# Performance work log

Hardware: AMD Instinct MI355X
Metric: run time of the kernel (lower is better)

The kernel has to match this reference:

```python
import jax, jax.numpy as jnp
import numpy as np

N_NODES = 50000
N_EDGES = 1000000
IN_C = 64
OUT_C = 64
N_TYPES = 4


def setup_inputs() -> dict:
    key = jax.random.key(0)
    k_x, k_ei, k_et, k_w, k_rw, k_rb = jax.random.split(key, 6)
    x = jax.random.normal(k_x, (N_NODES, IN_C), dtype=jnp.float32)
    edge_index = jax.random.randint(k_ei, (2, N_EDGES), 0, N_NODES, dtype=jnp.int64)
    edge_type = jax.random.randint(k_et, (N_EDGES,), 0, N_TYPES, dtype=jnp.int64)
    # xavier_uniform for weight: bound = sqrt(6/(in+out))
    bound_w = float(np.sqrt(6.0 / (IN_C + OUT_C)))
    weight = jax.random.uniform(k_w, (N_TYPES, IN_C, OUT_C), minval=-bound_w, maxval=bound_w, dtype=jnp.float32)
    # nn.Linear default init: kaiming_uniform-ish, U(-1/sqrt(in), 1/sqrt(in))
    bound_l = float(1.0 / np.sqrt(IN_C))
    root_w = jax.random.uniform(k_rw, (IN_C, OUT_C), minval=-bound_l, maxval=bound_l, dtype=jnp.float32)
    root_b = jax.random.uniform(k_rb, (OUT_C,), minval=-bound_l, maxval=bound_l, dtype=jnp.float32)
    return {"x": x, "edge_index": edge_index, "edge_type": edge_type,
            "weight": weight, "root_w": root_w, "root_b": root_b}


def reference(x, edge_index, edge_type, weight, root_w, root_b):
    src, dst = edge_index[0], edge_index[1]
    x_src = x[src]                                   # [E, in]
    # Per-type GEMM + masked select; avoids materializing weight[edge_type] ([E,in,out]).
    msgs = jnp.zeros((x_src.shape[0], weight.shape[2]), dtype=x.dtype)
    for t in range(weight.shape[0]):                 # small fixed type count
        sel = (edge_type == t)[:, None]
        msgs = msgs + jnp.where(sel, x_src @ weight[t], 0.0)
    # Scatter-add messages to destination nodes.
    agg = jax.ops.segment_sum(msgs, dst, num_segments=x.shape[0])  # [N, out]
    return agg + x @ root_w + root_b
```

## Files before the change

kernel.cpp:

```cpp
#include <hip/hip_runtime.h>

#define NT 64
#define NBMAX 4096
#define CAPB 2048
#define FILLB 256

typedef short bf16x8 __attribute__((ext_vector_type(8)));
typedef float f32x4  __attribute__((ext_vector_type(4)));

__device__ __forceinline__ unsigned short f2bf(float f) {
    unsigned u = __builtin_bit_cast(unsigned, f);
    unsigned r = (u + 0x7fffu + ((u >> 16) & 1u)) >> 16;
    return (unsigned short)r;
}
__device__ __forceinline__ float bf2f(unsigned short h) {
    return __builtin_bit_cast(float, (unsigned)h << 16);
}
__device__ __forceinline__ unsigned pack2(float a, float b) {
    return (unsigned)f2bf(a) | ((unsigned)f2bf(b) << 16);
}

__global__ __launch_bounds__(256) void prep_w_kernel(
    const float* __restrict__ weight, const float* __restrict__ root_w,
    unsigned short* __restrict__ wt, int* __restrict__ cursor, int nb)
{
    int g = blockIdx.x * 256 + threadIdx.x;
    if (g <= nb) cursor[g] = 0;
    if (g >= 5 * 4096) return;
    int m = g >> 12, rem = g & 4095, c = rem >> 6, k = rem & 63;
    float v = (m < 4) ? weight[m * 4096 + k * 64 + c] : root_w[k * 64 + c];
    int byte = m * 8192 + c * 128 + ((k * 2) ^ ((c & 7) << 4));
    wt[byte >> 1] = f2bf(v);
}

__global__ __launch_bounds__(256) void fused_fg_kernel(
    const float* __restrict__ x, const uint4* __restrict__ wt4,
    const float* __restrict__ root_b,
    float* __restrict__ out, unsigned short* __restrict__ y, int n_nodes,
    const int* __restrict__ ei, const int* __restrict__ et,
    int* __restrict__ cursor, int* __restrict__ spill,
    unsigned* __restrict__ payload, int n_edges, int nb, int ssh, int tsh)
{
    __shared__ __align__(16) char smem[49152];
    const int tid = threadIdx.x;

    if (blockIdx.x < FILLB) {
        int* lh    = (int*)smem;
        int* lbase = lh + NBMAX;
        const int chunk = (n_edges + FILLB - 1) / FILLB;
        const int lo = blockIdx.x * chunk;
        const int hi = min(lo + chunk, n_edges);
        for (int i = tid; i < nb; i += 256) lh[i] = 0;
        __syncthreads();
        for (int e = lo + tid; e < hi; e += 256)
            atomicAdd(&lh[ei[n_edges + e] >> 6], 1);
        __syncthreads();
        for (int i = tid; i < nb; i += 256) {
            int c = lh[i];
            lbase[i] = c ? atomicAdd(&cursor[i], c) : 0;
            lh[i] = 0;
        }
        __syncthreads();
        for (int e = lo + tid; e < hi; e += 256) {
            int src = ei[e];
            int d   = ei[n_edges + e];
            int t   = et[e];
            int b   = d >> 6;
            int r   = atomicAdd(&lh[b], 1);
            int pos = lbase[b] + r;
            if (pos < CAPB) {
                payload[(size_t)b * CAPB + pos] =
                    (unsigned)src | ((unsigned)(d & 63) << ssh) | ((unsigned)t << tsh);
            } else {
                int sp = atomicAdd(&cursor[nb], 1);
                spill[sp] = e;
            }
        }
        return;
    }

    uint4* lds4 = (uint4*)smem;
    const int node0 = (blockIdx.x - FILLB) * 64;

    for (int i = tid; i < 2560; i += 256) lds4[512 + i] = wt4[i];

    {
        int n    = tid >> 2;
        int kq   = tid & 3;
        int node = node0 + n;
        uint4 p0, p1;
        if (node < n_nodes) {
            const float4* src = reinterpret_cast<const float4*>(x)
                                + (size_t)node * 16 + kq * 4;
            float4 f0 = src[0], f1 = src[1], f2 = src[2], f3 = src[3];
            p0.x = pack2(f0.x, f0.y); p0.y = pack2(f0.z, f0.w);
            p0.z = pack2(f1.x, f1.y); p0.w = pack2(f1.z, f1.w);
            p1.x = pack2(f2.x, f2.y); p1.y = pack2(f2.z, f2.w);
            p1.z = pack2(f3.x, f3.y); p1.w = pack2(f3.z, f3.w);
        } else {
            p0 = make_uint4(0, 0, 0, 0);
            p1 = p0;
        }
        int s0 = (kq * 2) ^ (n & 7);
        lds4[n * 8 + s0]       = p0;
        lds4[n * 8 + (s0 ^ 1)] = p1;
    }
    __syncthreads();

    const int wv = tid >> 6;
    const int l  = tid & 63;
    const int lo = l & 15;
    const int hi = l >> 4;

    const int arow = wv * 16 + lo;
    bf16x8 a0 = *reinterpret_cast<const bf16x8*>(
        &lds4[arow * 8 + ((0 + hi) ^ (arow & 7))]);
    bf16x8 a1 = *reinterpret_cast<const bf16x8*>(
        &lds4[arow * 8 + ((4 + hi) ^ (arow & 7))]);

    for (int m = 0; m < 5; ++m) {
        f32x4 acc[4];
        #pragma unroll
        for (int ct = 0; ct < 4; ++ct)
            acc[ct] = (f32x4){0.f, 0.f, 0.f, 0.f};

        #pragma unroll
        for (int ct = 0; ct < 4; ++ct) {
            int c     = ct * 16 + lo;
            int bbase = 512 + m * 512 + c * 8;
            bf16x8 b0 = *reinterpret_cast<const bf16x8*>(
                &lds4[bbase + ((0 + hi) ^ (c & 7))]);
            acc[ct] = __builtin_amdgcn_mfma_f32_16x16x32_bf16(a0, b0, acc[ct], 0, 0, 0);
            bf16x8 b1 = *reinterpret_cast<const bf16x8*>(
                &lds4[bbase + ((4 + hi) ^ (c & 7))]);
            acc[ct] = __builtin_amdgcn_mfma_f32_16x16x32_bf16(a1, b1, acc[ct], 0, 0, 0);
        }

        if (m < 4) {
            unsigned short* __restrict__ ym = y + (size_t)m * n_nodes * 64;
            #pragma unroll
            for (int ct = 0; ct < 4; ++ct) {
                int col = ct * 16 + lo;
                #pragma unroll
                for (int r = 0; r < 4; ++r) {
                    int node = node0 + wv * 16 + hi * 4 + r;
                    if (node < n_nodes)
                        ym[(size_t)node * 64 + col] = f2bf(acc[ct][r]);
                }
            }
        } else {
            #pragma unroll
            for (int ct = 0; ct < 4; ++ct) {
                int col = ct * 16 + lo;
                float rb = root_b[col];
                #pragma unroll
                for (int r = 0; r < 4; ++r) {
                    int node = node0 + wv * 16 + hi * 4 + r;
                    if (node < n_nodes)
                        out[(size_t)node * 64 + col] = acc[ct][r] + rb;
                }
            }
        }
    }
}

__global__ __launch_bounds__(1024) void gatherb3_kernel(
    const int* __restrict__ cursor, const unsigned* __restrict__ payload,
    const int* __restrict__ spill, const int* __restrict__ ei,
    const int* __restrict__ et,
    const unsigned short* __restrict__ y, float* __restrict__ out,
    int n_nodes, int n_edges, int nb, int ssh, int tsh)
{
    __shared__ unsigned raw[CAPB];
    __shared__ unsigned srt[CAPB];
    __shared__ int hist[64];
    __shared__ int hoff[65];

    const int tid = threadIdx.x;
    const int b   = blockIdx.x;
    const int n_in = min(cursor[b], CAPB);
    const unsigned* __restrict__ pl_base = payload + (size_t)b * CAPB;

    if (tid < 64) hist[tid] = 0;
    __syncthreads();
    for (int i = tid; i < n_in; i += 1024) {
        unsigned pl = pl_base[i];
        raw[i] = pl;
        atomicAdd(&hist[(pl >> ssh) & 63], 1);
    }
    __syncthreads();
    if (tid < 64) {
        int v = hist[tid];
        int s = v;
        #pragma unroll
        for (int d = 1; d < 64; d <<= 1) {
            int u = __shfl_up(s, d, 64);
            if (tid >= d) s += u;
        }
        hoff[tid] = s - v;
        if (tid == 63) hoff[64] = s;
        hist[tid] = 0;
    }
    __syncthreads();
    for (int i = tid; i < n_in; i += 1024) {
        unsigned pl = raw[i];
        int lnode = (pl >> ssh) & 63;
        int r = atomicAdd(&hist[lnode], 1);
        srt[hoff[lnode] + r] = pl;
    }
    __syncthreads();

    const int g    = tid >> 4;
    const int cq   = tid & 15;
    const int node = b * 64 + g;
    const unsigned smask = (1u << ssh) - 1;
    const ushort4* __restrict__ y4 = reinterpret_cast<const ushort4*>(y);

    float4 acc = make_float4(0.f, 0.f, 0.f, 0.f);
    const int s0 = hoff[g];
    const int s1 = hoff[g + 1];
    int p = s0;
    for (; p + 1 < s1; p += 2) {
        unsigned pl0 = srt[p];
        unsigned pl1 = srt[p + 1];
        ushort4 v0 = y4[((long)(pl0 >> tsh) * n_nodes + (pl0 & smask)) * 16 + cq];
        ushort4 v1 = y4[((long)(pl1 >> tsh) * n_nodes + (pl1 & smask)) * 16 + cq];
        acc.x += bf2f(v0.x) + bf2f(v1.x);
        acc.y += bf2f(v0.y) + bf2f(v1.y);
        acc.z += bf2f(v0.z) + bf2f(v1.z);
        acc.w += bf2f(v0.w) + bf2f(v1.w);
    }
    if (p < s1) {
        unsigned pl = srt[p];
        ushort4 v = y4[((long)(pl >> tsh) * n_nodes + (pl & smask)) * 16 + cq];
        acc.x += bf2f(v.x); acc.y += bf2f(v.y);
        acc.z += bf2f(v.z); acc.w += bf2f(v.w);
    }

    const int S = cursor[nb];
    for (int i = 0; i < S; ++i) {
        int e = spill[i];
        int d = ei[n_edges + e];
        if ((d >> 6) == b && (d & 63) == g) {
            int src = ei[e];
            int t   = et[e];
            ushort4 v = y4[((long)t * n_nodes + src) * 16 + cq];
            acc.x += bf2f(v.x); acc.y += bf2f(v.y);
            acc.z += bf2f(v.z); acc.w += bf2f(v.w);
        }
    }

    if (node < n_nodes) {
        float4* o  = reinterpret_cast<float4*>(out) + (long)node * 16 + cq;
        float4 cur = *o;
        cur.x += acc.x; cur.y += acc.y; cur.z += acc.z; cur.w += acc.w;
        *o = cur;
    }
}

__global__ __launch_bounds__(256) void gemm_fused2_kernel(
    const float* __restrict__ x, const float* __restrict__ weight,
    const float* __restrict__ root_w, const float* __restrict__ root_b,
    float* __restrict__ out, unsigned short* __restrict__ y, int n_nodes)
{
    __shared__ unsigned short xsT[64][72];
    __shared__ float ws[64][72];
    const int tid   = threadIdx.x;
    const int node0 = blockIdx.x * 64;
    #pragma unroll
    for (int i = 0; i < 4; ++i) {
        int v    = tid + i * 256;
        int r    = v >> 4;
        int cq   = v & 15;
        int node = node0 + r;
        float4 x4 = (node < n_nodes)
                        ? reinterpret_cast<const float4*>(x)[(size_t)node * 16 + cq]
                        : make_float4(0.f, 0.f, 0.f, 0.f);
        xsT[cq * 4 + 0][r] = f2bf(x4.x);
        xsT[cq * 4 + 1][r] = f2bf(x4.y);
        xsT[cq * 4 + 2][r] = f2bf(x4.z);
        xsT[cq * 4 + 3][r] = f2bf(x4.w);
    }
    const int ng = tid & 31;
    const int cg = tid >> 5;
    float bias[8];
    #pragma unroll
    for (int j = 0; j < 8; ++j) bias[j] = root_b[cg * 8 + j];
    for (int m = 0; m < 5; ++m) {
        const float* __restrict__ W = (m < 4) ? (weight + m * 4096) : root_w;
        __syncthreads();
        #pragma unroll
        for (int i = 0; i < 4; ++i) {
            int v  = tid + i * 256;
            int r  = v >> 4;
            int cq = v & 15;
            float4 w4 = reinterpret_cast<const float4*>(W)[v];
            ws[r][cq * 4 + 0] = w4.x; ws[r][cq * 4 + 1] = w4.y;
            ws[r][cq * 4 + 2] = w4.z; ws[r][cq * 4 + 3] = w4.w;
        }
        __syncthreads();
        float acc[2][8];
        #pragma unroll
        for (int i = 0; i < 2; ++i)
            #pragma unroll
            for (int j = 0; j < 8; ++j) acc[i][j] = 0.f;
        #pragma unroll 4
        for (int k = 0; k < 64; ++k) {
            unsigned xu = *reinterpret_cast<const unsigned*>(&xsT[k][ng * 2]);
            float xv0 = __builtin_bit_cast(float, xu << 16);
            float xv1 = __builtin_bit_cast(float, xu & 0xffff0000u);
            float4 wa = *reinterpret_cast<const float4*>(&ws[k][cg * 8]);
            float4 wb = *reinterpret_cast<const float4*>(&ws[k][cg * 8 + 4]);
            float wv[8] = {wa.x, wa.y, wa.z, wa.w, wb.x, wb.y, wb.z, wb.w};
            #pragma unroll
            for (int j = 0; j < 8; ++j) {
                acc[0][j] += xv0 * wv[j];
                acc[1][j] += xv1 * wv[j];
            }
        }
        #pragma unroll
        for (int i = 0; i < 2; ++i) {
            int node = node0 + ng * 2 + i;
            if (node >= n_nodes) continue;
            if (m < 4) {
                uint4 o;
                o.x = pack2(acc[i][0], acc[i][1]);
                o.y = pack2(acc[i][2], acc[i][3]);
                o.z = pack2(acc[i][4], acc[i][5]);
                o.w = pack2(acc[i][6], acc[i][7]);
                *reinterpret_cast<uint4*>(
                    &y[((size_t)m * n_nodes + node) * 64 + cg * 8]) = o;
            } else {
                float4 oa = make_float4(acc[i][0] + bias[0], acc[i][1] + bias[1],
                                        acc[i][2] + bias[2], acc[i][3] + bias[3]);
                float4 ob = make_float4(acc[i][4] + bias[4], acc[i][5] + bias[5],
                                        acc[i][6] + bias[6], acc[i][7] + bias[7]);
                reinterpret_cast<float4*>(&out[(size_t)node * 64 + cg * 8])[0] = oa;
                reinterpret_cast<float4*>(&out[(size_t)node * 64 + cg * 8])[1] = ob;
            }
        }
    }
}

__global__ __launch_bounds__(256) void scatter_kernel(
    const int* __restrict__ ei, const int* __restrict__ et,
    const unsigned short* __restrict__ y, float* __restrict__ out,
    int n_edges, int n_nodes)
{
    long idx = (long)blockIdx.x * blockDim.x + threadIdx.x;
    if (idx >= (long)n_edges * 16) return;
    int e  = (int)(idx >> 4);
    int cq = (int)(idx & 15);
    int src  = ei[e];
    int dstn = ei[n_edges + e];
    int t    = et[e];
    ushort4 v = reinterpret_cast<const ushort4*>(y)[((long)t * n_nodes + src) * 16 + cq];
    float* o = out + (long)dstn * 64 + cq * 4;
    atomicAdd(o + 0, bf2f(v.x));
    atomicAdd(o + 1, bf2f(v.y));
    atomicAdd(o + 2, bf2f(v.z));
    atomicAdd(o + 3, bf2f(v.w));
}

__global__ __launch_bounds__(256) void gemm_root_kernel(
    const float* __restrict__ x, const float* __restrict__ root_w,
    const float* __restrict__ root_b, float* __restrict__ out, int n_nodes)
{
    __shared__ float xs[NT][65];
    __shared__ float ws[64][65];
    const int tid   = threadIdx.x;
    const int node0 = blockIdx.x * NT;
    #pragma unroll
    for (int i = 0; i < 4; ++i) {
        int v  = tid + i * 256;
        int r  = v >> 4;
        int cq = v & 15;
        float4 w4 = reinterpret_cast<const float4*>(root_w)[v];
        ws[r][cq * 4 + 0] = w4.x; ws[r][cq * 4 + 1] = w4.y;
        ws[r][cq * 4 + 2] = w4.z; ws[r][cq * 4 + 3] = w4.w;
        int node = node0 + r;
        float4 x4 = (node < n_nodes)
                        ? reinterpret_cast<const float4*>(x)[node * 16 + cq]
                        : make_float4(0.f, 0.f, 0.f, 0.f);
        xs[r][cq * 4 + 0] = x4.x; xs[r][cq * 4 + 1] = x4.y;
        xs[r][cq * 4 + 2] = x4.z; xs[r][cq * 4 + 3] = x4.w;
    }
    __syncthreads();
    const int tc = (tid & 15) * 4;
    const int tr = (tid >> 4) * 4;
    float acc[4][4];
    #pragma unroll
    for (int i = 0; i < 4; ++i)
        #pragma unroll
        for (int j = 0; j < 4; ++j) acc[i][j] = 0.f;
    #pragma unroll 4
    for (int k = 0; k < 64; ++k) {
        float xv[4], wv[4];
        #pragma unroll
        for (int i = 0; i < 4; ++i) xv[i] = xs[tr + i][k];
        #pragma unroll
        for (int j = 0; j < 4; ++j) wv[j] = ws[k][tc + j];
        #pragma unroll
        for (int i = 0; i < 4; ++i)
            #pragma unroll
            for (int j = 0; j < 4; ++j) acc[i][j] += xv[i] * wv[j];
    }
    #pragma unroll
    for (int i = 0; i < 4; ++i) {
        int node = node0 + tr + i;
        if (node < n_nodes) {
            float4 o = make_float4(acc[i][0] + root_b[tc + 0], acc[i][1] + root_b[tc + 1],
                                   acc[i][2] + root_b[tc + 2], acc[i][3] + root_b[tc + 3]);
            reinterpret_cast<float4*>(out)[node * 16 + (tc >> 2)] = o;
        }
    }
}

__global__ __launch_bounds__(256) void edge_direct_kernel(
    const float* __restrict__ x, const int* __restrict__ ei,
    const int* __restrict__ et, const float* __restrict__ weight,
    float* __restrict__ out, int n_edges)
{
    int gwave  = (int)((blockIdx.x * (long)blockDim.x + threadIdx.x) >> 6);
    int lane   = threadIdx.x & 63;
    int nwaves = (int)(((long)gridDim.x * blockDim.x) >> 6);
    for (int e = gwave; e < n_edges; e += nwaves) {
        int src  = ei[e];
        int dstn = ei[n_edges + e];
        int t    = et[e];
        float xv = x[src * 64 + lane];
        const float* __restrict__ W = weight + t * 4096;
        float acc = 0.f;
        #pragma unroll 8
        for (int k = 0; k < 64; ++k) {
            float xk = __shfl(xv, k);
            acc += xk * W[k * 64 + lane];
        }
        atomicAdd(&out[(long)dstn * 64 + lane], acc);
    }
}

extern "C" void kernel_launch(void* const* d_in, const int* in_sizes, int n_in,
                              void* d_out, int out_size, void* d_ws, size_t ws_size,
                              hipStream_t stream) {
    const float* x      = (const float*)d_in[0];
    const int*   ei     = (const int*)d_in[1];
    const int*   et     = (const int*)d_in[2];
    const float* weight = (const float*)d_in[3];
    const float* root_w = (const float*)d_in[4];
    const float* root_b = (const float*)d_in[5];
    float* out = (float*)d_out;

    const int n_nodes = in_sizes[0] / 64;
    const int n_edges = in_sizes[2];
    const int nb      = (n_nodes + 63) >> 6;

    int ssh = 1;
    while ((1 << ssh) < n_nodes) ++ssh;
    const int tsh = ssh + 6;

    const size_t wt_bytes = 5 * 4096 * sizeof(unsigned short);
    const size_t y_bytes  = (size_t)4 * n_nodes * 64 * sizeof(unsigned short);
    const size_t b_bytes  = wt_bytes + y_bytes +
        ((size_t)nb + 1 + (size_t)nb * CAPB + n_edges) * 4;

    if (nb <= NBMAX && tsh + 2 <= 32 && ws_size >= b_bytes) {
        unsigned short* wt      = (unsigned short*)d_ws;
        unsigned short* y       = (unsigned short*)((char*)d_ws + wt_bytes);
        int*            cursor  = (int*)((char*)d_ws + wt_bytes + y_bytes);
        unsigned*       payload = (unsigned*)(cursor + nb + 1);
        int*            spill   = (int*)(payload + (size_t)nb * CAPB);

        prep_w_kernel<<<80, 256, 0, stream>>>(weight, root_w, wt, cursor, nb);
        fused_fg_kernel<<<FILLB + nb, 256, 0, stream>>>(
            x, (const uint4*)wt, root_b, out, y, n_nodes,
            ei, et, cursor, spill, payload, n_edges, nb, ssh, tsh);
        gatherb3_kernel<<<nb, 1024, 0, stream>>>(
            cursor, payload, spill, ei, et, y, out,
            n_nodes, n_edges, nb, ssh, tsh);
    } else if (ws_size >= y_bytes) {
        unsigned short* y = (unsigned short*)d_ws;
        gemm_fused2_kernel<<<(n_nodes + 63) / 64, 256, 0, stream>>>(
            x, weight, root_w, root_b, out, y, n_nodes);
        long total  = (long)n_edges * 16;
        int  blocks = (int)((total + 255) / 256);
        scatter_kernel<<<blocks, 256, 0, stream>>>(ei, et, y, out, n_edges, n_nodes);
    } else {
        gemm_root_kernel<<<(n_nodes + NT - 1) / NT, 256, 0, stream>>>(
            x, root_w, root_b, out, n_nodes);
        edge_direct_kernel<<<4096, 256, 0, stream>>>(x, ei, et, weight, out, n_edges);
    }
}
```

Before: 66.99 us.

## Split fused fill/GEMM kernel and transpose MFMA operands for vectorized stores

Splits the combined edge-bucketing and per-node GEMM kernel into two separate launches, with the fill kernel now using 512 blocks instead of 256. The GEMM swaps the MFMA operand order so each lane holds four consecutive output columns of one node. That lets the y writes become packed 8-byte stores and the out writes become float4 stores with a vector bias load. The aim is to cut scattered 2-byte and 4-byte global stores and rebalance the fill work, at the cost of an extra kernel launch and losing overlap between fill and GEMM.

```diff
diff --git a/kernel.cpp b/kernel.cpp
--- a/kernel.cpp
+++ b/kernel.cpp
@@ -3,7 +3,6 @@
 #define NT 64
 #define NBMAX 4096
 #define CAPB 2048
-#define FILLB 256
 
 typedef short bf16x8 __attribute__((ext_vector_type(8)));
 typedef float f32x4  __attribute__((ext_vector_type(4)));
@@ -33,54 +32,54 @@
     wt[byte >> 1] = f2bf(v);
 }
 
-__global__ __launch_bounds__(256) void fused_fg_kernel(
+__global__ __launch_bounds__(256) void fillb_kernel(
+    const int* __restrict__ ei, const int* __restrict__ et,
+    int* __restrict__ cursor, int* __restrict__ spill,
+    unsigned* __restrict__ payload,
+    int n_edges, int nb, int ssh, int tsh)
+{
+    __shared__ int lh[NBMAX];
+    __shared__ int lbase[NBMAX];
+    const int chunk = (n_edges + gridDim.x - 1) / gridDim.x;
+    const int lo = blockIdx.x * chunk;
+    const int hi = min(lo + chunk, n_edges);
+    for (int i = threadIdx.x; i < nb; i += 256) lh[i] = 0;
+    __syncthreads();
+    for (int e = lo + threadIdx.x; e < hi; e += 256)
+        atomicAdd(&lh[ei[n_edges + e] >> 6], 1);
+    __syncthreads();
+    for (int i = threadIdx.x; i < nb; i += 256) {
+        int c = lh[i];
+        lbase[i] = c ? atomicAdd(&cursor[i], c) : 0;
+        lh[i] = 0;
+    }
+    __syncthreads();
+    for (int e = lo + threadIdx.x; e < hi; e += 256) {
+        int src = ei[e];
+        int d   = ei[n_edges + e];
+        int t   = et[e];
+        int b   = d >> 6;
+        int r   = atomicAdd(&lh[b], 1);
+        int pos = lbase[b] + r;
+        if (pos < CAPB) {
+            payload[(size_t)b * CAPB + pos] =
+                (unsigned)src | ((unsigned)(d & 63) << ssh) | ((unsigned)t << tsh);
+        } else {
+            int sp = atomicAdd(&cursor[nb], 1);
+            spill[sp] = e;
+        }
+    }
+}
+
+__global__ __launch_bounds__(256) void gemm_mfma2_kernel(
     const float* __restrict__ x, const uint4* __restrict__ wt4,
     const float* __restrict__ root_b,
-    float* __restrict__ out, unsigned short* __restrict__ y, int n_nodes,
-    const int* __restrict__ ei, const int* __restrict__ et,
-    int* __restrict__ cursor, int* __restrict__ spill,
-    unsigned* __restrict__ payload, int n_edges, int nb, int ssh, int tsh)
-{
-    __shared__ __align__(16) char smem[49152];
-    const int tid = threadIdx.x;
-
-    if (blockIdx.x < FILLB) {
-        int* lh    = (int*)smem;
-        int* lbase = lh + NBMAX;
-        const int chunk = (n_edges + FILLB - 1) / FILLB;
-        const int lo = blockIdx.x * chunk;
-        const int hi = min(lo + chunk, n_edges);
-        for (int i = tid; i < nb; i += 256) lh[i] = 0;
-        __syncthreads();
-        for (int e = lo + tid; e < hi; e += 256)
-            atomicAdd(&lh[ei[n_edges + e] >> 6], 1);
-        __syncthreads();
-        for (int i = tid; i < nb; i += 256) {
-            int c = lh[i];
-            lbase[i] = c ? atomicAdd(&cursor[i], c) : 0;
-            lh[i] = 0;
-        }
-        __syncthreads();
-        for (int e = lo + tid; e < hi; e += 256) {
-            int src = ei[e];
-            int d   = ei[n_edges + e];
-            int t   = et[e];
-            int b   = d >> 6;
-            int r   = atomicAdd(&lh[b], 1);
-            int pos = lbase[b] + r;
-            if (pos < CAPB) {
-                payload[(size_t)b * CAPB + pos] =
-                    (unsigned)src | ((unsigned)(d & 63) << ssh) | ((unsigned)t << tsh);
-            } else {
-                int sp = atomicAdd(&cursor[nb], 1);
-                spill[sp] = e;
-            }
-        }
-        return;
-    }
-
-    uint4* lds4 = (uint4*)smem;
-    const int node0 = (blockIdx.x - FILLB) * 64;
+    float* __restrict__ out, unsigned short* __restrict__ y, int n_nodes)
+{
+    __shared__ uint4 lds4[3072];
+
+    const int tid   = threadIdx.x;
+    const int node0 = blockIdx.x * 64;
 
     for (int i = tid; i < 2560; i += 256) lds4[512 + i] = wt4[i];
 
@@ -113,51 +112,53 @@
     const int hi = l >> 4;
 
     const int arow = wv * 16 + lo;
-    bf16x8 a0 = *reinterpret_cast<const bf16x8*>(
+    bf16x8 xb0 = *reinterpret_cast<const bf16x8*>(
         &lds4[arow * 8 + ((0 + hi) ^ (arow & 7))]);
-    bf16x8 a1 = *reinterpret_cast<const bf16x8*>(
+    bf16x8 xb1 = *reinterpret_cast<const bf16x8*>(
         &lds4[arow * 8 + ((4 + hi) ^ (arow & 7))]);
+
+    const int node   = node0 + wv * 16 + lo;
+    const bool valid = (node < n_nodes);
 
     for (int m = 0; m < 5; ++m) {
         f32x4 acc[4];
         #pragma unroll
-        for (int ct = 0; ct < 4; ++ct)
-            acc[ct] = (f32x4){0.f, 0.f, 0.f, 0.f};
-
-        #pragma unroll
-        for (int ct = 0; ct < 4; ++ct) {
-            int c     = ct * 16 + lo;
+        for (int j = 0; j < 4; ++j)
+            acc[j] = (f32x4){0.f, 0.f, 0.f, 0.f};
+
+        #pragma unroll
+        for (int j = 0; j < 4; ++j) {
+            int c     = j * 16 + lo;
             int bbase = 512 + m * 512 + c * 8;
-            bf16x8 b0 = *reinterpret_cast<const bf16x8*>(
+            bf16x8 w0 = *reinterpret_cast<const bf16x8*>(
                 &lds4[bbase + ((0 + hi) ^ (c & 7))]);
-            acc[ct] = __builtin_amdgcn_mfma_f32_16x16x32_bf16(a0, b0, acc[ct], 0, 0, 0);
-            bf16x8 b1 = *reinterpret_cast<const bf16x8*>(
+            acc[j] = __builtin_amdgcn_mfma_f32_16x16x32_bf16(w0, xb0, acc[j], 0, 0, 0);
+            bf16x8 w1 = *reinterpret_cast<const bf16x8*>(
                 &lds4[bbase + ((4 + hi) ^ (c & 7))]);
-            acc[ct] = __builtin_amdgcn_mfma_f32_16x16x32_bf16(a1, b1, acc[ct], 0, 0, 0);
+            acc[j] = __builtin_amdgcn_mfma_f32_16x16x32_bf16(w1, xb1, acc[j], 0, 0, 0);
         }
 
         if (m < 4) {
-            unsigned short* __restrict__ ym = y + (size_t)m * n_nodes * 64;
-            #pragma unroll
-            for (int ct = 0; ct < 4; ++ct) {
-                int col = ct * 16 + lo;
+            if (valid) {
+                unsigned short* __restrict__ ym = y + (size_t)m * n_nodes * 64;
                 #pragma unroll
-                for (int r = 0; r < 4; ++r) {
-                    int node = node0 + wv * 16 + hi * 4 + r;
-                    if (node < n_nodes)
-                        ym[(size_t)node * 64 + col] = f2bf(acc[ct][r]);
+                for (int j = 0; j < 4; ++j) {
+                    uint2 o;
+                    o.x = pack2(acc[j][0], acc[j][1]);
+                    o.y = pack2(acc[j][2], acc[j][3]);
+                    *reinterpret_cast<uint2*>(
+                        &ym[(size_t)node * 64 + j * 16 + hi * 4]) = o;
                 }
             }
         } else {
-            #pragma unroll
-            for (int ct = 0; ct < 4; ++ct) {
-                int col = ct * 16 + lo;
-                float rb = root_b[col];
+            if (valid) {
                 #pragma unroll
-                for (int r = 0; r < 4; ++r) {
-                    int node = node0 + wv * 16 + hi * 4 + r;
-                    if (node < n_nodes)
-                        out[(size_t)node * 64 + col] = acc[ct][r] + rb;
+                for (int j = 0; j < 4; ++j) {
+                    float4 rb = reinterpret_cast<const float4*>(root_b)[j * 4 + hi];
+                    float4 o  = make_float4(acc[j][0] + rb.x, acc[j][1] + rb.y,
+                                            acc[j][2] + rb.z, acc[j][3] + rb.w);
+                    *reinterpret_cast<float4*>(
+                        &out[(size_t)node * 64 + j * 16 + hi * 4]) = o;
                 }
             }
         }
@@ -472,9 +473,10 @@
         int*            spill   = (int*)(payload + (size_t)nb * CAPB);
 
         prep_w_kernel<<<80, 256, 0, stream>>>(weight, root_w, wt, cursor, nb);
-        fused_fg_kernel<<<FILLB + nb, 256, 0, stream>>>(
-            x, (const uint4*)wt, root_b, out, y, n_nodes,
-            ei, et, cursor, spill, payload, n_edges, nb, ssh, tsh);
+        fillb_kernel<<<512, 256, 0, stream>>>(ei, et, cursor, spill,
+                                              payload, n_edges, nb, ssh, tsh);
+        gemm_mfma2_kernel<<<nb, 256, 0, stream>>>(x, (const uint4*)wt, root_b,
+                                                  out, y, n_nodes);
         gatherb3_kernel<<<nb, 1024, 0, stream>>>(
             cursor, payload, spill, ei, et, y, out,
             n_nodes, n_edges, nb, ssh, tsh);
```

Measured after the change: 81.72 us. +22.0%, slower.
